# Kernel tuning notes

Measured on AMD Instinct MI355X. Metric: run time of the kernel, lower is better.

The kernel has to match this reference:

```python
import jax, jax.numpy as jnp
import numpy as np

EPS = 1e-6
B, T, D, A = 16, 2048, 512, 128
SCALE = A ** (-0.5)


def _xavier(key, fan_in, fan_out):
    limit = np.sqrt(6.0 / (fan_in + fan_out)).astype(np.float32)
    return jax.random.uniform(key, (fan_in, fan_out), jnp.float32, -limit, limit)


def setup_inputs() -> dict:
    key = jax.random.key(0)
    kx, kq, kk, kv = jax.random.split(key, 4)
    x = jax.random.normal(kx, (B, T, D), jnp.float32)
    Wq = _xavier(kq, D, A)
    Wk = _xavier(kk, D, A)
    Wv = _xavier(kv, D, 1)
    bq = jnp.full((A,), 0.01, jnp.float32)
    bk = jnp.full((A,), 0.01, jnp.float32)
    bv = jnp.full((1,), 0.01, jnp.float32)
    return {"x": x, "Wq": Wq, "bq": bq, "Wk": Wk, "bk": bk, "Wv": Wv, "bv": bv}


def reference(x, Wq, bq, Wk, bk, Wv, bv):
    # mean-variance norm over features (torch.std default is unbiased -> ddof=1)
    mu = jnp.mean(x, axis=-1, keepdims=True)
    sd = jnp.std(x, axis=-1, keepdims=True, ddof=1)
    xn = (x - mu) / (sd + EPS)
    Q = xn @ Wq + bq            # [B, T, A]
    K = xn @ Wk + bk            # [B, T, A]
    V = xn @ Wv + bv            # [B, T, 1]
    scores = jnp.einsum("bta,bsa->bts", Q, K) * SCALE  # [B, T, T]
    w_att = jax.nn.softmax(scores, axis=-1)
    w = jnp.einsum("bts,bso->bto", w_att, V)           # [B, T, 1]
    return (w, w_att)
```

## Files before the change

### kernel.cpp

```cpp
#include <hip/hip_runtime.h>

#define NB 16
#define NT 2048
#define ND 512
#define NA 128
#define EPSV 1e-6f
#define SCALE 0.08838834764831845f
#define NCH 4
#define SCH 512

typedef __bf16 bf16;
typedef __bf16 bf16x4 __attribute__((ext_vector_type(4)));
typedef __bf16 bf16x8 __attribute__((ext_vector_type(8)));
typedef float f32x4 __attribute__((ext_vector_type(4)));

__global__ void prep_wt(const float* __restrict__ Wq, const float* __restrict__ Wk,
                        bf16* __restrict__ WT) {
    int n = blockIdx.x;
    const float* W = (n < NA) ? Wq : Wk;
    int col = n & (NA - 1);
    for (int k = threadIdx.x; k < ND; k += blockDim.x)
        WT[(size_t)n * ND + k] = (bf16)W[(size_t)k * NA + col];
}

__launch_bounds__(256)
__global__ void norm_proj(const float* __restrict__ x, const float* __restrict__ Wv,
                          const float* __restrict__ bvp, const bf16* __restrict__ WT,
                          const float* __restrict__ bq, const float* __restrict__ bk,
                          bf16* __restrict__ QK, float* __restrict__ Vout) {
    __shared__ bf16 xn[16 * ND];
    const int tid = threadIdx.x;
    const int lane = tid & 63, wv = tid >> 6;
    const int row0 = blockIdx.x * 16;

    float wvv[8];
    float sumw = 0.f;
#pragma unroll
    for (int i = 0; i < 4; ++i) { wvv[i]     = Wv[lane * 4 + i];       sumw += wvv[i]; }
#pragma unroll
    for (int i = 0; i < 4; ++i) { wvv[4 + i] = Wv[256 + lane * 4 + i]; sumw += wvv[4 + i]; }
#pragma unroll
    for (int m = 1; m < 64; m <<= 1) sumw += __shfl_xor(sumw, m);
    const float bvs = bvp[0];

#pragma unroll
    for (int r = 0; r < 4; ++r) {
        const int lrow = wv * 4 + r;
        const int grow = row0 + lrow;
        const float* xr = x + (size_t)grow * ND;
        f32x4 a = *(const f32x4*)(xr + lane * 4);
        f32x4 b = *(const f32x4*)(xr + 256 + lane * 4);
        float s = 0.f, sq = 0.f, dw = 0.f;
#pragma unroll
        for (int i = 0; i < 4; ++i) { s += a[i]; sq += a[i] * a[i]; dw += a[i] * wvv[i]; }
#pragma unroll
        for (int i = 0; i < 4; ++i) { s += b[i]; sq += b[i] * b[i]; dw += b[i] * wvv[4 + i]; }
#pragma unroll
        for (int m = 1; m < 64; m <<= 1) {
            s  += __shfl_xor(s, m);
            sq += __shfl_xor(sq, m);
            dw += __shfl_xor(dw, m);
        }
        const float mu  = s * (1.f / 512.f);
        float var = (sq - 512.f * mu * mu) * (1.f / 511.f);
        var = fmaxf(var, 0.f);
        const float inv = 1.f / (sqrtf(var) + EPSV);
        if (lane == 0) Vout[grow] = (dw - mu * sumw) * inv + bvs;

        const int sw = (lrow & 7) << 4;
        bf16x4 v0, v1;
#pragma unroll
        for (int i = 0; i < 4; ++i) v0[i] = (bf16)((a[i] - mu) * inv);
#pragma unroll
        for (int i = 0; i < 4; ++i) v1[i] = (bf16)((b[i] - mu) * inv);
        *(bf16x4*)((char*)xn + lrow * 1024 + ((lane * 8) ^ sw))       = v0;
        *(bf16x4*)((char*)xn + lrow * 1024 + ((512 + lane * 8) ^ sw)) = v1;
    }
    __syncthreads();

    const int c = lane & 15, g = lane >> 4;
    const int asw = (c & 7) << 4;
    f32x4 acc[4];
#pragma unroll
    for (int i = 0; i < 4; ++i) acc[i] = f32x4{0.f, 0.f, 0.f, 0.f};

    for (int ks = 0; ks < 16; ++ks) {
        const bf16x8 af = *(const bf16x8*)((const char*)xn + c * 1024 +
                                           ((ks * 64 + g * 16) ^ asw));
#pragma unroll
        for (int i = 0; i < 4; ++i) {
            const int n = wv * 64 + i * 16 + c;
            const bf16x8 bfr = *(const bf16x8*)(WT + (size_t)n * ND + ks * 32 + g * 8);
            acc[i] = __builtin_amdgcn_mfma_f32_16x16x32_bf16(af, bfr, acc[i], 0, 0, 0);
        }
    }
#pragma unroll
    for (int i = 0; i < 4; ++i) {
        const int n = wv * 64 + i * 16 + c;
        const float bias = (n < NA) ? bq[n] : bk[n - NA];
#pragma unroll
        for (int j = 0; j < 4; ++j)
            QK[(size_t)(row0 + g * 4 + j) * 256 + n] = (bf16)(acc[i][j] + bias);
    }
}

__launch_bounds__(256)
__global__ void attn_pass1(const bf16* __restrict__ QK, const float* __restrict__ Vg,
                           float* __restrict__ pl, float* __restrict__ pw) {
    __shared__ bf16 Kt[64 * NA];
    const int tid = threadIdx.x;
    const int lane = tid & 63, wv = tid >> 6;
    const int b = blockIdx.z, t0 = blockIdx.x * 64, sc = blockIdx.y;
    const int c = lane & 15, g = lane >> 4;
    const int trow = t0 + wv * 16 + c;

    bf16x8 qf[4];
    const bf16* qrow = QK + (size_t)(b * NT + trow) * 256;
#pragma unroll
    for (int ks = 0; ks < 4; ++ks) qf[ks] = *(const bf16x8*)(qrow + ks * 32 + g * 8);

    const int srow = tid >> 4, scc = tid & 15;
    const bf16* kbase = QK + (size_t)(b * NT + sc * SCH + srow) * 256 + NA + scc * 8;
    bf16* kdst = (bf16*)((char*)Kt + srow * 256 + ((scc * 16) ^ ((srow & 7) << 4)));
    bf16x8 sreg[4];

#pragma unroll
    for (int i = 0; i < 4; ++i)
        sreg[i] = *(const bf16x8*)(kbase + (size_t)(i * 16) * 256);
#pragma unroll
    for (int i = 0; i < 4; ++i)
        *(bf16x8*)((char*)kdst + i * 16 * 256) = sreg[i];
    __syncthreads();

    const float* vbase = Vg + b * NT + sc * SCH;
    float l_loc = 0.f, w_loc = 0.f;

    for (int tt = 0; tt < SCH / 64; ++tt) {
        if (tt + 1 < SCH / 64) {
#pragma unroll
            for (int i = 0; i < 4; ++i)
                sreg[i] = *(const bf16x8*)(kbase + (size_t)((tt + 1) * 64 + i * 16) * 256);
        }

#pragma unroll
        for (int ns = 0; ns < 4; ++ns) {
            f32x4 acc = f32x4{0.f, 0.f, 0.f, 0.f};
            const int rr = ns * 16 + c;
            const int rsw = (rr & 7) << 4;
#pragma unroll
            for (int ks = 0; ks < 4; ++ks) {
                const bf16x8 afr = *(const bf16x8*)((const char*)Kt + rr * 256 +
                                                    ((ks * 64 + g * 16) ^ rsw));
                acc = __builtin_amdgcn_mfma_f32_16x16x32_bf16(afr, qf[ks], acc, 0, 0, 0);
            }
            const f32x4 vv = *(const f32x4*)(vbase + tt * 64 + ns * 16 + g * 4);
#pragma unroll
            for (int jj = 0; jj < 4; ++jj) {
                const float p = __expf(acc[jj] * SCALE);
                l_loc += p;
                w_loc += p * vv[jj];
            }
        }

        if (tt + 1 < SCH / 64) {
            __syncthreads();
#pragma unroll
            for (int i = 0; i < 4; ++i)
                *(bf16x8*)((char*)kdst + i * 16 * 256) = sreg[i];
            __syncthreads();
        }
    }

#pragma unroll
    for (int mask = 16; mask <= 32; mask <<= 1) {
        l_loc += __shfl_xor(l_loc, mask);
        w_loc += __shfl_xor(w_loc, mask);
    }
    if (g == 0) {
        const int idx = sc * (NB * NT) + b * NT + trow;
        pl[idx] = l_loc;
        pw[idx] = w_loc;
    }
}

__launch_bounds__(256)
__global__ void attn_pass2(const bf16* __restrict__ QK, const float* __restrict__ pl,
                           const float* __restrict__ pw, float* __restrict__ out_w,
                           float* __restrict__ out_att) {
    __shared__ bf16 Kt[64 * NA];
    const int tid = threadIdx.x;
    const int lane = tid & 63, wv = tid >> 6;
    const int b = blockIdx.z, t0 = blockIdx.x * 64, sc = blockIdx.y;
    const int c = lane & 15, g = lane >> 4;
    const int trow = t0 + wv * 16 + c;

    bf16x8 qf[4];
    const bf16* qrow = QK + (size_t)(b * NT + trow) * 256;
#pragma unroll
    for (int ks = 0; ks < 4; ++ks) qf[ks] = *(const bf16x8*)(qrow + ks * 32 + g * 8);

    float L = 0.f, W = 0.f;
#pragma unroll
    for (int ch = 0; ch < NCH; ++ch) {
        L += pl[ch * (NB * NT) + b * NT + trow];
        W += pw[ch * (NB * NT) + b * NT + trow];
    }
    const float lrow = 1.f / L;
    if (sc == 0 && g == 0) out_w[b * NT + trow] = W * lrow;

    float* orow = out_att + (size_t)(b * NT + trow) * NT;

    const int srow = tid >> 4, scc = tid & 15;
    const bf16* kbase = QK + (size_t)(b * NT + sc * SCH + srow) * 256 + NA + scc * 8;
    bf16* kdst = (bf16*)((char*)Kt + srow * 256 + ((scc * 16) ^ ((srow & 7) << 4)));
    bf16x8 sreg[4];

#pragma unroll
    for (int i = 0; i < 4; ++i)
        sreg[i] = *(const bf16x8*)(kbase + (size_t)(i * 16) * 256);
#pragma unroll
    for (int i = 0; i < 4; ++i)
        *(bf16x8*)((char*)kdst + i * 16 * 256) = sreg[i];
    __syncthreads();

    for (int tt = 0; tt < SCH / 64; ++tt) {
        if (tt + 1 < SCH / 64) {
#pragma unroll
            for (int i = 0; i < 4; ++i)
                sreg[i] = *(const bf16x8*)(kbase + (size_t)((tt + 1) * 64 + i * 16) * 256);
        }

        const int s0 = sc * SCH + tt * 64;
#pragma unroll
        for (int ns = 0; ns < 4; ++ns) {
            f32x4 acc = f32x4{0.f, 0.f, 0.f, 0.f};
            const int rr = ns * 16 + c;
            const int rsw = (rr & 7) << 4;
#pragma unroll
            for (int ks = 0; ks < 4; ++ks) {
                const bf16x8 afr = *(const bf16x8*)((const char*)Kt + rr * 256 +
                                                    ((ks * 64 + g * 16) ^ rsw));
                acc = __builtin_amdgcn_mfma_f32_16x16x32_bf16(afr, qf[ks], acc, 0, 0, 0);
            }
            f32x4 w;
#pragma unroll
            for (int jj = 0; jj < 4; ++jj)
                w[jj] = __expf(acc[jj] * SCALE) * lrow;
            *(f32x4*)(orow + s0 + ns * 16 + g * 4) = w;
        }

        if (tt + 1 < SCH / 64) {
            __syncthreads();
#pragma unroll
            for (int i = 0; i < 4; ++i)
                *(bf16x8*)((char*)kdst + i * 16 * 256) = sreg[i];
            __syncthreads();
        }
    }
}

extern "C" void kernel_launch(void* const* d_in, const int* in_sizes, int n_in,
                              void* d_out, int out_size, void* d_ws, size_t ws_size,
                              hipStream_t stream) {
    const float* x  = (const float*)d_in[0];
    const float* Wq = (const float*)d_in[1];
    const float* bq = (const float*)d_in[2];
    const float* Wk = (const float*)d_in[3];
    const float* bk = (const float*)d_in[4];
    const float* Wv = (const float*)d_in[5];
    const float* bv = (const float*)d_in[6];

    float* out_w   = (float*)d_out;
    float* out_att = (float*)d_out + NB * NT;

    char* ws = (char*)d_ws;
    bf16*  WT = (bf16*)ws;
    float* V  = (float*)(ws + 262144);
    bf16*  QK = (bf16*)(ws + 393216);
    float* pl = (float*)(ws + 17170432);
    float* pw = (float*)(ws + 17694720);

    prep_wt<<<dim3(256), dim3(256), 0, stream>>>(Wq, Wk, WT);
    norm_proj<<<dim3((NB * NT) / 16), dim3(256), 0, stream>>>(x, Wv, bv, WT, bq, bk, QK, V);
    attn_pass1<<<dim3(NT / 64, NCH, NB), dim3(256), 0, stream>>>(QK, V, pl, pw);
    attn_pass2<<<dim3(NT / 64, NCH, NB), dim3(256), 0, stream>>>(QK, pl, pw, out_w, out_att);
}
```

Before: 173.9 us.

## Switch attention passes to 32x32x16 MFMA tiles with 2x2 wave layout

Both attention passes now compute each 64x64 score tile with 32x32x16 bf16 MFMA instructions instead of 16x16x32, arranging the four waves as a 2x2 grid over query and key rows. The LDS swizzle for K is widened to match the new access pattern. In pass 1 the per-row partial sums are combined across waves through shared memory. The aim is fewer MFMA and LDS instructions per tile, at the cost of a different output store pattern and an extra barrier in pass 1.

```diff
diff --git a/kernel.cpp b/kernel.cpp
--- a/kernel.cpp
+++ b/kernel.cpp
@@ -13,6 +13,7 @@
 typedef __bf16 bf16x4 __attribute__((ext_vector_type(4)));
 typedef __bf16 bf16x8 __attribute__((ext_vector_type(8)));
 typedef float f32x4 __attribute__((ext_vector_type(4)));
+typedef float f32x16 __attribute__((ext_vector_type(16)));
 
 __global__ void prep_wt(const float* __restrict__ Wq, const float* __restrict__ Wk,
                         bf16* __restrict__ WT) {
@@ -108,20 +109,22 @@
 __global__ void attn_pass1(const bf16* __restrict__ QK, const float* __restrict__ Vg,
                            float* __restrict__ pl, float* __restrict__ pw) {
     __shared__ bf16 Kt[64 * NA];
+    __shared__ float redl[4][32], redw[4][32];
     const int tid = threadIdx.x;
-    const int lane = tid & 63, wv = tid >> 6;
+    const int lane = tid & 63, w = tid >> 6;
     const int b = blockIdx.z, t0 = blockIdx.x * 64, sc = blockIdx.y;
-    const int c = lane & 15, g = lane >> 4;
-    const int trow = t0 + wv * 16 + c;
-
-    bf16x8 qf[4];
-    const bf16* qrow = QK + (size_t)(b * NT + trow) * 256;
-#pragma unroll
-    for (int ks = 0; ks < 4; ++ks) qf[ks] = *(const bf16x8*)(qrow + ks * 32 + g * 8);
+    const int j = lane & 31, h = lane >> 5;
+    const int th = w >> 1, sh = w & 1;
+    const int tcol = t0 + th * 32 + j;
+
+    bf16x8 qf[8];
+    const bf16* qrow = QK + (size_t)(b * NT + tcol) * 256;
+#pragma unroll
+    for (int ks = 0; ks < 8; ++ks) qf[ks] = *(const bf16x8*)(qrow + ks * 16 + h * 8);
 
     const int srow = tid >> 4, scc = tid & 15;
     const bf16* kbase = QK + (size_t)(b * NT + sc * SCH + srow) * 256 + NA + scc * 8;
-    bf16* kdst = (bf16*)((char*)Kt + srow * 256 + ((scc * 16) ^ ((srow & 7) << 4)));
+    bf16* kdst = (bf16*)((char*)Kt + srow * 256 + ((scc * 16) ^ (srow << 4)));
     bf16x8 sreg[4];
 
 #pragma unroll
@@ -133,6 +136,9 @@
     __syncthreads();
 
     const float* vbase = Vg + b * NT + sc * SCH;
+    const int rr = sh * 32 + j;
+    const int rsw = (rr & 15) << 4;
+    const char* abase = (const char*)Kt + rr * 256;
     float l_loc = 0.f, w_loc = 0.f;
 
     for (int tt = 0; tt < SCH / 64; ++tt) {
@@ -142,24 +148,21 @@
                 sreg[i] = *(const bf16x8*)(kbase + (size_t)((tt + 1) * 64 + i * 16) * 256);
         }
 
-#pragma unroll
-        for (int ns = 0; ns < 4; ++ns) {
-            f32x4 acc = f32x4{0.f, 0.f, 0.f, 0.f};
-            const int rr = ns * 16 + c;
-            const int rsw = (rr & 7) << 4;
-#pragma unroll
-            for (int ks = 0; ks < 4; ++ks) {
-                const bf16x8 afr = *(const bf16x8*)((const char*)Kt + rr * 256 +
-                                                    ((ks * 64 + g * 16) ^ rsw));
-                acc = __builtin_amdgcn_mfma_f32_16x16x32_bf16(afr, qf[ks], acc, 0, 0, 0);
+        f32x16 acc = (f32x16)(0.0f);
+#pragma unroll
+        for (int ks = 0; ks < 8; ++ks) {
+            const bf16x8 af = *(const bf16x8*)(abase + ((ks * 32 + h * 16) ^ rsw));
+            acc = __builtin_amdgcn_mfma_f32_32x32x16_bf16(af, qf[ks], acc, 0, 0, 0);
+        }
+#pragma unroll
+        for (int q = 0; q < 4; ++q) {
+            const f32x4 vv = *(const f32x4*)(vbase + tt * 64 + sh * 32 + 8 * q + 4 * h);
+#pragma unroll
+            for (int r = 0; r < 4; ++r) {
+                const float p = __expf(acc[4 * q + r] * SCALE);
+                l_loc += p;
+                w_loc += p * vv[r];
             }
-            const f32x4 vv = *(const f32x4*)(vbase + tt * 64 + ns * 16 + g * 4);
-#pragma unroll
-            for (int jj = 0; jj < 4; ++jj) {
-                const float p = __expf(acc[jj] * SCALE);
-                l_loc += p;
-                w_loc += p * vv[jj];
-            }
         }
 
         if (tt + 1 < SCH / 64) {
@@ -171,15 +174,20 @@
         }
     }
 
-#pragma unroll
-    for (int mask = 16; mask <= 32; mask <<= 1) {
-        l_loc += __shfl_xor(l_loc, mask);
-        w_loc += __shfl_xor(w_loc, mask);
-    }
-    if (g == 0) {
-        const int idx = sc * (NB * NT) + b * NT + trow;
-        pl[idx] = l_loc;
-        pw[idx] = w_loc;
+    l_loc += __shfl_xor(l_loc, 32);
+    w_loc += __shfl_xor(w_loc, 32);
+    if (h == 0) {
+        redl[w][j] = l_loc;
+        redw[w][j] = w_loc;
+    }
+    __syncthreads();
+    if (tid < 64) {
+        const int tth = tid >> 5, tj = tid & 31;
+        const float L = redl[tth * 2][tj] + redl[tth * 2 + 1][tj];
+        const float W = redw[tth * 2][tj] + redw[tth * 2 + 1][tj];
+        const int idx = sc * (NB * NT) + b * NT + t0 + tid;
+        pl[idx] = L;
+        pw[idx] = W;
     }
 }
 
@@ -189,30 +197,29 @@
                            float* __restrict__ out_att) {
     __shared__ bf16 Kt[64 * NA];
     const int tid = threadIdx.x;
-    const int lane = tid & 63, wv = tid >> 6;
+    const int lane = tid & 63, w = tid >> 6;
     const int b = blockIdx.z, t0 = blockIdx.x * 64, sc = blockIdx.y;
-    const int c = lane & 15, g = lane >> 4;
-    const int trow = t0 + wv * 16 + c;
-
-    bf16x8 qf[4];
-    const bf16* qrow = QK + (size_t)(b * NT + trow) * 256;
-#pragma unroll
-    for (int ks = 0; ks < 4; ++ks) qf[ks] = *(const bf16x8*)(qrow + ks * 32 + g * 8);
+    const int j = lane & 31, h = lane >> 5;
+    const int th = w >> 1, sh = w & 1;
+    const int tcol = t0 + th * 32 + j;
+
+    bf16x8 qf[8];
+    const bf16* qrow = QK + (size_t)(b * NT + tcol) * 256;
+#pragma unroll
+    for (int ks = 0; ks < 8; ++ks) qf[ks] = *(const bf16x8*)(qrow + ks * 16 + h * 8);
 
     float L = 0.f, W = 0.f;
 #pragma unroll
     for (int ch = 0; ch < NCH; ++ch) {
-        L += pl[ch * (NB * NT) + b * NT + trow];
-        W += pw[ch * (NB * NT) + b * NT + trow];
+        L += pl[ch * (NB * NT) + b * NT + tcol];
+        W += pw[ch * (NB * NT) + b * NT + tcol];
     }
     const float lrow = 1.f / L;
-    if (sc == 0 && g == 0) out_w[b * NT + trow] = W * lrow;
-
-    float* orow = out_att + (size_t)(b * NT + trow) * NT;
+    if (sc == 0 && sh == 0 && h == 0) out_w[b * NT + tcol] = W * lrow;
 
     const int srow = tid >> 4, scc = tid & 15;
     const bf16* kbase = QK + (size_t)(b * NT + sc * SCH + srow) * 256 + NA + scc * 8;
-    bf16* kdst = (bf16*)((char*)Kt + srow * 256 + ((scc * 16) ^ ((srow & 7) << 4)));
+    bf16* kdst = (bf16*)((char*)Kt + srow * 256 + ((scc * 16) ^ (srow << 4)));
     bf16x8 sreg[4];
 
 #pragma unroll
@@ -223,6 +230,11 @@
         *(bf16x8*)((char*)kdst + i * 16 * 256) = sreg[i];
     __syncthreads();
 
+    const int rr = sh * 32 + j;
+    const int rsw = (rr & 15) << 4;
+    const char* abase = (const char*)Kt + rr * 256;
+    float* orow = out_att + (size_t)(b * NT + tcol) * NT;
+
     for (int tt = 0; tt < SCH / 64; ++tt) {
         if (tt + 1 < SCH / 64) {
 #pragma unroll
@@ -230,23 +242,20 @@
                 sreg[i] = *(const bf16x8*)(kbase + (size_t)((tt + 1) * 64 + i * 16) * 256);
         }
 
-        const int s0 = sc * SCH + tt * 64;
-#pragma unroll
-        for (int ns = 0; ns < 4; ++ns) {
-            f32x4 acc = f32x4{0.f, 0.f, 0.f, 0.f};
-            const int rr = ns * 16 + c;
-            const int rsw = (rr & 7) << 4;
-#pragma unroll
-            for (int ks = 0; ks < 4; ++ks) {
-                const bf16x8 afr = *(const bf16x8*)((const char*)Kt + rr * 256 +
-                                                    ((ks * 64 + g * 16) ^ rsw));
-                acc = __builtin_amdgcn_mfma_f32_16x16x32_bf16(afr, qf[ks], acc, 0, 0, 0);
-            }
-            f32x4 w;
-#pragma unroll
-            for (int jj = 0; jj < 4; ++jj)
-                w[jj] = __expf(acc[jj] * SCALE) * lrow;
-            *(f32x4*)(orow + s0 + ns * 16 + g * 4) = w;
+        f32x16 acc = (f32x16)(0.0f);
+#pragma unroll
+        for (int ks = 0; ks < 8; ++ks) {
+            const bf16x8 af = *(const bf16x8*)(abase + ((ks * 32 + h * 16) ^ rsw));
+            acc = __builtin_amdgcn_mfma_f32_32x32x16_bf16(af, qf[ks], acc, 0, 0, 0);
+        }
+        const int s0 = sc * SCH + tt * 64 + sh * 32 + 4 * h;
+#pragma unroll
+        for (int q = 0; q < 4; ++q) {
+            f32x4 w4;
+#pragma unroll
+            for (int r = 0; r < 4; ++r)
+                w4[r] = __expf(acc[4 * q + r] * SCALE) * lrow;
+            *(f32x4*)(orow + s0 + 8 * q) = w4;
         }
 
         if (tt + 1 < SCH / 64) {
```

Measured after the change: 182.6 us. +5.0%, slower.

## Tile attention waves as 2x2 over query and key rows to cut LDS reads

Applied to the files above, without the earlier changes.

Each wave in both attention passes now covers 32 query rows and 32 key rows instead of 16 query rows and all 64 key rows of a tile. Key fragments loaded from LDS are held in registers and reused for two query groups, which halves LDS read traffic per MFMA. Pass 1 gains a small shared-memory reduction so the two key-half waves can combine their partial sums. This costs more registers for the query and key fragments, which may lower occupancy.

```diff
diff --git a/kernel.cpp b/kernel.cpp
--- a/kernel.cpp
+++ b/kernel.cpp
@@ -108,16 +108,21 @@
 __global__ void attn_pass1(const bf16* __restrict__ QK, const float* __restrict__ Vg,
                            float* __restrict__ pl, float* __restrict__ pw) {
     __shared__ bf16 Kt[64 * NA];
+    __shared__ float redl[4][32], redw[4][32];
     const int tid = threadIdx.x;
-    const int lane = tid & 63, wv = tid >> 6;
+    const int lane = tid & 63, w = tid >> 6;
     const int b = blockIdx.z, t0 = blockIdx.x * 64, sc = blockIdx.y;
     const int c = lane & 15, g = lane >> 4;
-    const int trow = t0 + wv * 16 + c;
-
-    bf16x8 qf[4];
-    const bf16* qrow = QK + (size_t)(b * NT + trow) * 256;
-#pragma unroll
-    for (int ks = 0; ks < 4; ++ks) qf[ks] = *(const bf16x8*)(qrow + ks * 32 + g * 8);
+    const int th = w >> 1, sh = w & 1;
+
+    bf16x8 qf[2][4];
+#pragma unroll
+    for (int tg = 0; tg < 2; ++tg) {
+        const bf16* qrow = QK + (size_t)(b * NT + t0 + th * 32 + tg * 16 + c) * 256;
+#pragma unroll
+        for (int ks = 0; ks < 4; ++ks)
+            qf[tg][ks] = *(const bf16x8*)(qrow + ks * 32 + g * 8);
+    }
 
     const int srow = tid >> 4, scc = tid & 15;
     const bf16* kbase = QK + (size_t)(b * NT + sc * SCH + srow) * 256 + NA + scc * 8;
@@ -133,7 +138,7 @@
     __syncthreads();
 
     const float* vbase = Vg + b * NT + sc * SCH;
-    float l_loc = 0.f, w_loc = 0.f;
+    float l_loc[2] = {0.f, 0.f}, w_loc[2] = {0.f, 0.f};
 
     for (int tt = 0; tt < SCH / 64; ++tt) {
         if (tt + 1 < SCH / 64) {
@@ -142,23 +147,33 @@
                 sreg[i] = *(const bf16x8*)(kbase + (size_t)((tt + 1) * 64 + i * 16) * 256);
         }
 
-#pragma unroll
-        for (int ns = 0; ns < 4; ++ns) {
-            f32x4 acc = f32x4{0.f, 0.f, 0.f, 0.f};
-            const int rr = ns * 16 + c;
+        bf16x8 af[2][4];
+#pragma unroll
+        for (int sg = 0; sg < 2; ++sg) {
+            const int rr = sh * 32 + sg * 16 + c;
             const int rsw = (rr & 7) << 4;
-#pragma unroll
-            for (int ks = 0; ks < 4; ++ks) {
-                const bf16x8 afr = *(const bf16x8*)((const char*)Kt + rr * 256 +
-                                                    ((ks * 64 + g * 16) ^ rsw));
-                acc = __builtin_amdgcn_mfma_f32_16x16x32_bf16(afr, qf[ks], acc, 0, 0, 0);
-            }
-            const f32x4 vv = *(const f32x4*)(vbase + tt * 64 + ns * 16 + g * 4);
-#pragma unroll
-            for (int jj = 0; jj < 4; ++jj) {
-                const float p = __expf(acc[jj] * SCALE);
-                l_loc += p;
-                w_loc += p * vv[jj];
+            const char* abase = (const char*)Kt + rr * 256;
+#pragma unroll
+            for (int ks = 0; ks < 4; ++ks)
+                af[sg][ks] = *(const bf16x8*)(abase + ((ks * 64 + g * 16) ^ rsw));
+        }
+
+#pragma unroll
+        for (int tg = 0; tg < 2; ++tg) {
+#pragma unroll
+            for (int sg = 0; sg < 2; ++sg) {
+                f32x4 acc = f32x4{0.f, 0.f, 0.f, 0.f};
+#pragma unroll
+                for (int ks = 0; ks < 4; ++ks)
+                    acc = __builtin_amdgcn_mfma_f32_16x16x32_bf16(af[sg][ks], qf[tg][ks],
+                                                                  acc, 0, 0, 0);
+                const f32x4 vv = *(const f32x4*)(vbase + tt * 64 + sh * 32 + sg * 16 + g * 4);
+#pragma unroll
+                for (int jj = 0; jj < 4; ++jj) {
+                    const float p = __expf(acc[jj] * SCALE);
+                    l_loc[tg] += p;
+                    w_loc[tg] += p * vv[jj];
+                }
             }
         }
 
@@ -172,14 +187,28 @@
     }
 
 #pragma unroll
-    for (int mask = 16; mask <= 32; mask <<= 1) {
-        l_loc += __shfl_xor(l_loc, mask);
-        w_loc += __shfl_xor(w_loc, mask);
+    for (int tg = 0; tg < 2; ++tg) {
+#pragma unroll
+        for (int mask = 16; mask <= 32; mask <<= 1) {
+            l_loc[tg] += __shfl_xor(l_loc[tg], mask);
+            w_loc[tg] += __shfl_xor(w_loc[tg], mask);
+        }
     }
     if (g == 0) {
-        const int idx = sc * (NB * NT) + b * NT + trow;
-        pl[idx] = l_loc;
-        pw[idx] = w_loc;
+#pragma unroll
+        for (int tg = 0; tg < 2; ++tg) {
+            redl[w][tg * 16 + c] = l_loc[tg];
+            redw[w][tg * 16 + c] = w_loc[tg];
+        }
+    }
+    __syncthreads();
+    if (tid < 64) {
+        const int th2 = tid >> 5, u = tid & 31;
+        const float L = redl[th2 * 2][u] + redl[th2 * 2 + 1][u];
+        const float W = redw[th2 * 2][u] + redw[th2 * 2 + 1][u];
+        const int idx = sc * (NB * NT) + b * NT + t0 + tid;
+        pl[idx] = L;
+        pw[idx] = W;
     }
 }
 
@@ -189,26 +218,29 @@
                            float* __restrict__ out_att) {
     __shared__ bf16 Kt[64 * NA];
     const int tid = threadIdx.x;
-    const int lane = tid & 63, wv = tid >> 6;
+    const int lane = tid & 63, w = tid >> 6;
     const int b = blockIdx.z, t0 = blockIdx.x * 64, sc = blockIdx.y;
     const int c = lane & 15, g = lane >> 4;
-    const int trow = t0 + wv * 16 + c;
-
-    bf16x8 qf[4];
-    const bf16* qrow = QK + (size_t)(b * NT + trow) * 256;
-#pragma unroll
-    for (int ks = 0; ks < 4; ++ks) qf[ks] = *(const bf16x8*)(qrow + ks * 32 + g * 8);
-
-    float L = 0.f, W = 0.f;
-#pragma unroll
-    for (int ch = 0; ch < NCH; ++ch) {
-        L += pl[ch * (NB * NT) + b * NT + trow];
-        W += pw[ch * (NB * NT) + b * NT + trow];
-    }
-    const float lrow = 1.f / L;
-    if (sc == 0 && g == 0) out_w[b * NT + trow] = W * lrow;
-
-    float* orow = out_att + (size_t)(b * NT + trow) * NT;
+    const int th = w >> 1, sh = w & 1;
+
+    bf16x8 qf[2][4];
+    float lrow[2];
+#pragma unroll
+    for (int tg = 0; tg < 2; ++tg) {
+        const int trow = t0 + th * 32 + tg * 16 + c;
+        const bf16* qrow = QK + (size_t)(b * NT + trow) * 256;
+#pragma unroll
+        for (int ks = 0; ks < 4; ++ks)
+            qf[tg][ks] = *(const bf16x8*)(qrow + ks * 32 + g * 8);
+        float L = 0.f, W = 0.f;
+#pragma unroll
+        for (int ch = 0; ch < NCH; ++ch) {
+            L += pl[ch * (NB * NT) + b * NT + trow];
+            W += pw[ch * (NB * NT) + b * NT + trow];
+        }
+        lrow[tg] = 1.f / L;
+        if (sc == 0 && sh == 0 && g == 0) out_w[b * NT + trow] = W * lrow[tg];
+    }
 
     const int srow = tid >> 4, scc = tid & 15;
     const bf16* kbase = QK + (size_t)(b * NT + sc * SCH + srow) * 256 + NA + scc * 8;
@@ -230,23 +262,33 @@
                 sreg[i] = *(const bf16x8*)(kbase + (size_t)((tt + 1) * 64 + i * 16) * 256);
         }
 
-        const int s0 = sc * SCH + tt * 64;
-#pragma unroll
-        for (int ns = 0; ns < 4; ++ns) {
-            f32x4 acc = f32x4{0.f, 0.f, 0.f, 0.f};
-            const int rr = ns * 16 + c;
+        bf16x8 af[2][4];
+#pragma unroll
+        for (int sg = 0; sg < 2; ++sg) {
+            const int rr = sh * 32 + sg * 16 + c;
             const int rsw = (rr & 7) << 4;
-#pragma unroll
-            for (int ks = 0; ks < 4; ++ks) {
-                const bf16x8 afr = *(const bf16x8*)((const char*)Kt + rr * 256 +
-                                                    ((ks * 64 + g * 16) ^ rsw));
-                acc = __builtin_amdgcn_mfma_f32_16x16x32_bf16(afr, qf[ks], acc, 0, 0, 0);
+            const char* abase = (const char*)Kt + rr * 256;
+#pragma unroll
+            for (int ks = 0; ks < 4; ++ks)
+                af[sg][ks] = *(const bf16x8*)(abase + ((ks * 64 + g * 16) ^ rsw));
+        }
+
+#pragma unroll
+        for (int tg = 0; tg < 2; ++tg) {
+            float* orow = out_att + (size_t)(b * NT + t0 + th * 32 + tg * 16 + c) * NT;
+#pragma unroll
+            for (int sg = 0; sg < 2; ++sg) {
+                f32x4 acc = f32x4{0.f, 0.f, 0.f, 0.f};
+#pragma unroll
+                for (int ks = 0; ks < 4; ++ks)
+                    acc = __builtin_amdgcn_mfma_f32_16x16x32_bf16(af[sg][ks], qf[tg][ks],
+                                                                  acc, 0, 0, 0);
+                f32x4 w4;
+#pragma unroll
+                for (int jj = 0; jj < 4; ++jj)
+                    w4[jj] = __expf(acc[jj] * SCALE) * lrow[tg];
+                *(f32x4*)(orow + sc * SCH + tt * 64 + sh * 32 + sg * 16 + g * 4) = w4;
             }
-            f32x4 w;
-#pragma unroll
-            for (int jj = 0; jj < 4; ++jj)
-                w[jj] = __expf(acc[jj] * SCALE) * lrow;
-            *(f32x4*)(orow + s0 + ns * 16 + g * 4) = w;
         }
 
         if (tt + 1 < SCH / 64) {
```

After: 176.9 us. Within noise of the previous version (+1.7%).

## Stream K tiles via global_load_lds into double-buffered LDS in attention passes

Applied to the files above, without the earlier changes.

Both attention passes now fetch K tiles with direct global-to-LDS loads instead of staging through registers. The loads go into a double-buffered shared tile of 32 rows instead of one 64-row buffer, so each iteration needs one barrier instead of two. The aim is to cut VGPR pressure and the register round trip, and to overlap the next tile's load with the current tile's MFMA work. The smaller tile doubles the iteration count and barriers per chunk. Correctness depends on the swizzled source addressing lining up with how the LDS reads are laid out.

```diff
diff --git a/kernel.cpp b/kernel.cpp
--- a/kernel.cpp
+++ b/kernel.cpp
@@ -8,11 +8,18 @@
 #define SCALE 0.08838834764831845f
 #define NCH 4
 #define SCH 512
+#define TR 32
 
 typedef __bf16 bf16;
 typedef __bf16 bf16x4 __attribute__((ext_vector_type(4)));
 typedef __bf16 bf16x8 __attribute__((ext_vector_type(8)));
 typedef float f32x4 __attribute__((ext_vector_type(4)));
+
+__device__ __forceinline__ void gll16(const void* g, void* l) {
+    __builtin_amdgcn_global_load_lds(
+        (const __attribute__((address_space(1))) void*)g,
+        (__attribute__((address_space(3))) void*)l, 16, 0, 0);
+}
 
 __global__ void prep_wt(const float* __restrict__ Wq, const float* __restrict__ Wk,
                         bf16* __restrict__ WT) {
@@ -107,53 +114,56 @@
 __launch_bounds__(256)
 __global__ void attn_pass1(const bf16* __restrict__ QK, const float* __restrict__ Vg,
                            float* __restrict__ pl, float* __restrict__ pw) {
-    __shared__ bf16 Kt[64 * NA];
+    __shared__ bf16 Kt[2][TR * NA];
     const int tid = threadIdx.x;
-    const int lane = tid & 63, wv = tid >> 6;
+    const int lane = tid & 63, w = tid >> 6;
     const int b = blockIdx.z, t0 = blockIdx.x * 64, sc = blockIdx.y;
     const int c = lane & 15, g = lane >> 4;
-    const int trow = t0 + wv * 16 + c;
+    const int trow = t0 + w * 16 + c;
 
     bf16x8 qf[4];
     const bf16* qrow = QK + (size_t)(b * NT + trow) * 256;
 #pragma unroll
     for (int ks = 0; ks < 4; ++ks) qf[ks] = *(const bf16x8*)(qrow + ks * 32 + g * 8);
 
-    const int srow = tid >> 4, scc = tid & 15;
-    const bf16* kbase = QK + (size_t)(b * NT + sc * SCH + srow) * 256 + NA + scc * 8;
-    bf16* kdst = (bf16*)((char*)Kt + srow * 256 + ((scc * 16) ^ ((srow & 7) << 4)));
-    bf16x8 sreg[4];
-
-#pragma unroll
-    for (int i = 0; i < 4; ++i)
-        sreg[i] = *(const bf16x8*)(kbase + (size_t)(i * 16) * 256);
-#pragma unroll
-    for (int i = 0; i < 4; ++i)
-        *(bf16x8*)((char*)kdst + i * 16 * 256) = sreg[i];
+    const int sr0 = w * 2;
+    const int lr = lane >> 4, cc = lane & 15;
+    const bf16* kch = QK + (size_t)(b * NT + sc * SCH) * 256 + NA;
+
+#pragma unroll
+    for (int i = 0; i < 2; ++i) {
+        const int r = (sr0 + i) * 4 + lr;
+        gll16(kch + (size_t)r * 256 + ((cc ^ (r & 7)) * 8),
+              (char*)Kt[0] + (sr0 + i) * 1024);
+    }
     __syncthreads();
 
     const float* vbase = Vg + b * NT + sc * SCH;
     float l_loc = 0.f, w_loc = 0.f;
 
-    for (int tt = 0; tt < SCH / 64; ++tt) {
-        if (tt + 1 < SCH / 64) {
-#pragma unroll
-            for (int i = 0; i < 4; ++i)
-                sreg[i] = *(const bf16x8*)(kbase + (size_t)((tt + 1) * 64 + i * 16) * 256);
-        }
-
-#pragma unroll
-        for (int ns = 0; ns < 4; ++ns) {
+    for (int tt = 0; tt < SCH / TR; ++tt) {
+        if (tt + 1 < SCH / TR) {
+#pragma unroll
+            for (int i = 0; i < 2; ++i) {
+                const int r = (sr0 + i) * 4 + lr;
+                gll16(kch + (size_t)((tt + 1) * TR + r) * 256 + ((cc ^ (r & 7)) * 8),
+                      (char*)Kt[(tt + 1) & 1] + (sr0 + i) * 1024);
+            }
+        }
+
+        const char* kt = (const char*)Kt[tt & 1];
+#pragma unroll
+        for (int ns = 0; ns < 2; ++ns) {
             f32x4 acc = f32x4{0.f, 0.f, 0.f, 0.f};
             const int rr = ns * 16 + c;
             const int rsw = (rr & 7) << 4;
 #pragma unroll
             for (int ks = 0; ks < 4; ++ks) {
-                const bf16x8 afr = *(const bf16x8*)((const char*)Kt + rr * 256 +
+                const bf16x8 afr = *(const bf16x8*)(kt + rr * 256 +
                                                     ((ks * 64 + g * 16) ^ rsw));
                 acc = __builtin_amdgcn_mfma_f32_16x16x32_bf16(afr, qf[ks], acc, 0, 0, 0);
             }
-            const f32x4 vv = *(const f32x4*)(vbase + tt * 64 + ns * 16 + g * 4);
+            const f32x4 vv = *(const f32x4*)(vbase + tt * TR + ns * 16 + g * 4);
 #pragma unroll
             for (int jj = 0; jj < 4; ++jj) {
                 const float p = __expf(acc[jj] * SCALE);
@@ -161,14 +171,7 @@
                 w_loc += p * vv[jj];
             }
         }
-
-        if (tt + 1 < SCH / 64) {
-            __syncthreads();
-#pragma unroll
-            for (int i = 0; i < 4; ++i)
-                *(bf16x8*)((char*)kdst + i * 16 * 256) = sreg[i];
-            __syncthreads();
-        }
+        __syncthreads();
     }
 
 #pragma unroll
@@ -187,12 +190,12 @@
 __global__ void attn_pass2(const bf16* __restrict__ QK, const float* __restrict__ pl,
                            const float* __restrict__ pw, float* __restrict__ out_w,
                            float* __restrict__ out_att) {
-    __shared__ bf16 Kt[64 * NA];
+    __shared__ bf16 Kt[2][TR * NA];
     const int tid = threadIdx.x;
-    const int lane = tid & 63, wv = tid >> 6;
+    const int lane = tid & 63, w = tid >> 6;
     const int b = blockIdx.z, t0 = blockIdx.x * 64, sc = blockIdx.y;
     const int c = lane & 15, g = lane >> 4;
-    const int trow = t0 + wv * 16 + c;
+    const int trow = t0 + w * 16 + c;
 
     bf16x8 qf[4];
     const bf16* qrow = QK + (size_t)(b * NT + trow) * 256;
@@ -208,54 +211,50 @@
     const float lrow = 1.f / L;
     if (sc == 0 && g == 0) out_w[b * NT + trow] = W * lrow;
 
+    const int sr0 = w * 2;
+    const int lr = lane >> 4, cc = lane & 15;
+    const bf16* kch = QK + (size_t)(b * NT + sc * SCH) * 256 + NA;
+
+#pragma unroll
+    for (int i = 0; i < 2; ++i) {
+        const int r = (sr0 + i) * 4 + lr;
+        gll16(kch + (size_t)r * 256 + ((cc ^ (r & 7)) * 8),
+              (char*)Kt[0] + (sr0 + i) * 1024);
+    }
+    __syncthreads();
+
     float* orow = out_att + (size_t)(b * NT + trow) * NT;
 
-    const int srow = tid >> 4, scc = tid & 15;
-    const bf16* kbase = QK + (size_t)(b * NT + sc * SCH + srow) * 256 + NA + scc * 8;
-    bf16* kdst = (bf16*)((char*)Kt + srow * 256 + ((scc * 16) ^ ((srow & 7) << 4)));
-    bf16x8 sreg[4];
-
-#pragma unroll
-    for (int i = 0; i < 4; ++i)
-        sreg[i] = *(const bf16x8*)(kbase + (size_t)(i * 16) * 256);
-#pragma unroll
-    for (int i = 0; i < 4; ++i)
-        *(bf16x8*)((char*)kdst + i * 16 * 256) = sreg[i];
-    __syncthreads();
-
-    for (int tt = 0; tt < SCH / 64; ++tt) {
-        if (tt + 1 < SCH / 64) {
-#pragma unroll
-            for (int i = 0; i < 4; ++i)
-                sreg[i] = *(const bf16x8*)(kbase + (size_t)((tt + 1) * 64 + i * 16) * 256);
-        }
-
-        const int s0 = sc * SCH + tt * 64;
-#pragma unroll
-        for (int ns = 0; ns < 4; ++ns) {
+    for (int tt = 0; tt < SCH / TR; ++tt) {
+        if (tt + 1 < SCH / TR) {
+#pragma unroll
+            for (int i = 0; i < 2; ++i) {
+                const int r = (sr0 + i) * 4 + lr;
+                gll16(kch + (size_t)((tt + 1) * TR + r) * 256 + ((cc ^ (r & 7)) * 8),
+                      (char*)Kt[(tt + 1) & 1] + (sr0 + i) * 1024);
+            }
+        }
+
+        const char* kt = (const char*)Kt[tt & 1];
+        const int s0 = sc * SCH + tt * TR;
+#pragma unroll
+        for (int ns = 0; ns < 2; ++ns) {
             f32x4 acc = f32x4{0.f, 0.f, 0.f, 0.f};
             const int rr = ns * 16 + c;
             const int rsw = (rr & 7) << 4;
 #pragma unroll
             for (int ks = 0; ks < 4; ++ks) {
-                const bf16x8 afr = *(const bf16x8*)((const char*)Kt + rr * 256 +
+                const bf16x8 afr = *(const bf16x8*)(kt + rr * 256 +
                                                     ((ks * 64 + g * 16) ^ rsw));
                 acc = __builtin_amdgcn_mfma_f32_16x16x32_bf16(afr, qf[ks], acc, 0, 0, 0);
             }
-            f32x4 w;
+            f32x4 w4;
 #pragma unroll
             for (int jj = 0; jj < 4; ++jj)
-                w[jj] = __expf(acc[jj] * SCALE) * lrow;
-            *(f32x4*)(orow + s0 + ns * 16 + g * 4) = w;
-        }
-
-        if (tt + 1 < SCH / 64) {
-            __syncthreads();
-#pragma unroll
-            for (int i = 0; i < 4; ++i)
-                *(bf16x8*)((char*)kdst + i * 16 * 256) = sreg[i];
-            __syncthreads();
-        }
+                w4[jj] = __expf(acc[jj] * SCALE) * lrow;
+            *(f32x4*)(orow + s0 + ns * 16 + g * 4) = w4;
+        }
+        __syncthreads();
     }
 }
 
```

Measured after the change: 176.4 us. No clear change (+1.4%).
